# Kernel tuning notes

Hardware: AMD Instinct MI355X
Metric: run time of the kernel (lower is better)

The kernel has to match this reference:

```python
import jax, jax.numpy as jnp
import numpy as np

N, E, F_IN, H, L, G = 50000, 800000, 128, 256, 64, 500


def setup_inputs() -> dict:
    key = jax.random.key(0)
    ks = jax.random.split(key, 12)
    s = 0.02
    x = jax.random.normal(ks[0], (N, F_IN), dtype=jnp.float32)
    edge_index = jax.random.randint(ks[1], (2, E), 0, N, dtype=jnp.int64 if jax.config.jax_enable_x64 else jnp.int32)
    batch = jnp.sort(jax.random.randint(ks[2], (N,), 0, G, dtype=jnp.int32))
    return {
        "x": x,
        "edge_index": edge_index,
        "batch": batch,
        "num_graphs": G,
        "W1": jax.random.normal(ks[3], (F_IN, H), dtype=jnp.float32) * s,
        "b1": jnp.zeros((H,), dtype=jnp.float32),
        "W2": jax.random.normal(ks[4], (H, H), dtype=jnp.float32) * s,
        "b2": jnp.zeros((H,), dtype=jnp.float32),
        "Wmu": jax.random.normal(ks[5], (H, L), dtype=jnp.float32) * s,
        "bmu": jnp.zeros((L,), dtype=jnp.float32),
        "Wlv": jax.random.normal(ks[6], (H, L), dtype=jnp.float32) * s,
        "blv": jnp.zeros((L,), dtype=jnp.float32),
    }


def _gcn_norm(edge_index, n_nodes):
    # PyG GCNConv default: add self-loops, symmetric normalization D^-1/2 A_hat D^-1/2
    loop = jnp.arange(n_nodes, dtype=edge_index.dtype)
    src = jnp.concatenate([edge_index[0], loop])
    dst = jnp.concatenate([edge_index[1], loop])
    deg = jax.ops.segment_sum(jnp.ones_like(dst, dtype=jnp.float32), dst, num_segments=n_nodes)
    dinv = jnp.where(deg > 0, jax.lax.rsqrt(deg), 0.0)
    norm = dinv[src] * dinv[dst]  # [E + N]
    return src, dst, norm


def _gcn_conv(h, src, dst, norm, W, b, n_nodes):
    h = h @ W                              # [N, out]
    msg = norm[:, None] * h[src]           # gather + scale: [E+N, out]
    agg = jax.ops.segment_sum(msg, dst, num_segments=n_nodes)  # scatter-add
    return agg + b


def reference(x, edge_index, batch, num_graphs, W1, b1, W2, b2, Wmu, bmu, Wlv, blv):
    n_nodes = x.shape[0]
    src, dst, norm = _gcn_norm(edge_index, n_nodes)
    h = jax.nn.relu(_gcn_conv(x, src, dst, norm, W1, b1, n_nodes))
    h = jax.nn.relu(_gcn_conv(h, src, dst, norm, W2, b2, n_nodes))
    # global_mean_pool over batch ids
    sums = jax.ops.segment_sum(h, batch, num_segments=num_graphs)       # [G, H]
    cnt = jax.ops.segment_sum(jnp.ones((n_nodes,), h.dtype), batch, num_segments=num_graphs)
    h_graph = sums / jnp.maximum(cnt, 1.0)[:, None]
    mu = h_graph @ Wmu + bmu
    logvar = h_graph @ Wlv + blv
    return mu, logvar
```

## Files before the change

### kernel.cpp

```cpp
#include <hip/hip_runtime.h>
#include <hip/hip_fp16.h>

#define N_NODES 50000
#define N_EDGES 800000
#define F_IN_D  128
#define H_DIM   256
#define L_DIM   64
#define G_NUM   500

typedef unsigned int   u32;
typedef unsigned short u16;
typedef unsigned char  u8;
typedef __attribute__((ext_vector_type(8))) short short8;
typedef __attribute__((ext_vector_type(4))) float f32x4;
typedef __attribute__((ext_vector_type(2))) float f32x2;

#define BSHIFT 8
#define NBUCK ((N_NODES + 255) >> BSHIFT)
#define CUR_STRIDE 16
#define BIN_NB 512
#define EPB ((N_EDGES + BIN_NB - 1) / BIN_NB)
#define BUCK_CAP 8192

static __device__ __forceinline__ float bf2f(u16 u) {
    union { u32 i; float f; } x; x.i = ((u32)u) << 16; return x.f;
}
static __device__ __forceinline__ u16 f2bf(float f) {
    union { float f; u32 i; } x; x.f = f;
    u32 r = (x.i + 0x7fffu + ((x.i >> 16) & 1u)) >> 16;
    return (u16)r;
}
static __device__ __forceinline__ float edge_w(u32 e) {
    return __half2float(__ushort_as_half((u16)(e >> 16)));
}

static __device__ __forceinline__ u32 pack4_fp8(u32 a, u32 b) {
    u32 w = __builtin_amdgcn_cvt_pk_fp8_f32(bf2f((u16)(a & 0xffff)),
                                            bf2f((u16)(a >> 16)), 0, false);
    w = __builtin_amdgcn_cvt_pk_fp8_f32(bf2f((u16)(b & 0xffff)),
                                        bf2f((u16)(b >> 16)), w, true);
    return w;
}

static __device__ __forceinline__ u32 bswz_idx(int n, int k, int plane, int KS) {
    int n0g = n >> 6, nt = (n >> 4) & 3, lr = n & 15;
    int k0i = k >> 5, ks = k & 31, lq = ks >> 3, j = ks & 7;
    return ((u32)((((n0g * KS + k0i) * 2 + plane) * 4 + nt) * 64 + lq * 16 + lr)) * 8 + j;
}

#define NXQ (N_NODES * F_IN_D / 4)
#define NW1 (F_IN_D * H_DIM)
#define NW2 (H_DIM * H_DIM)
#define NB_SCAN  ((N_NODES + 255) / 256)
#define NB_CONV  ((NXQ + NW1 + NW2 + 255) / 256)

__global__ void prep_kernel(const int* __restrict__ src, const int* __restrict__ dst,
                            const int* __restrict__ batch, int* __restrict__ goff,
                            const float* __restrict__ x, u8* __restrict__ xq,
                            const float* __restrict__ W1, u16* __restrict__ w1swz,
                            const float* __restrict__ W2, u16* __restrict__ w2swz,
                            int* __restrict__ bcur, u32* __restrict__ binrec) {
    int b = blockIdx.x;
    if (b < BIN_NB) {
        __shared__ int lhist[NBUCK];
        __shared__ int lbase[NBUCK];
        int t = threadIdx.x;
        int e0 = b * EPB;
        int e1 = e0 + EPB; if (e1 > N_EDGES) e1 = N_EDGES;
        for (int i = t; i < NBUCK; i += 256) lhist[i] = 0;
        __syncthreads();
        for (int e = e0 + t; e < e1; e += 256)
            atomicAdd(&lhist[dst[e] >> BSHIFT], 1);
        __syncthreads();
        for (int i = t; i < NBUCK; i += 256) {
            int c = lhist[i];
            lbase[i] = i * BUCK_CAP + (c ? atomicAdd(&bcur[i * CUR_STRIDE], c) : 0);
            lhist[i] = 0;
        }
        __syncthreads();
        for (int e = e0 + t; e < e1; e += 256) {
            int d = dst[e], s = src[e];
            int bkt = d >> BSHIFT;
            int rank = atomicAdd(&lhist[bkt], 1);
            binrec[(size_t)lbase[bkt] + rank] = (u32)s | ((u32)(d & 255) << 16);
        }
    } else if (b < BIN_NB + NB_SCAN) {
        int i = (b - BIN_NB) * 256 + threadIdx.x;
        if (i >= N_NODES) return;
        int v = batch[i];
        if (i == 0) {
            for (int g = 0; g <= v; ++g) goff[g] = 0;
        } else {
            int p = batch[i - 1];
            for (int g = p + 1; g <= v; ++g) goff[g] = i;
        }
        if (i == N_NODES - 1) {
            for (int g = v + 1; g <= G_NUM; ++g) goff[g] = N_NODES;
        }
    } else {
        int i = (b - BIN_NB - NB_SCAN) * 256 + threadIdx.x;
        if (i < NXQ) {
            float4 v = *(const float4*)&x[(size_t)i * 4];
            u32 w = __builtin_amdgcn_cvt_pk_fp8_f32(v.x, v.y, 0, false);
            w = __builtin_amdgcn_cvt_pk_fp8_f32(v.z, v.w, w, true);
            *(u32*)&xq[(size_t)i * 4] = w;
        } else if (i < NXQ + NW1) {
            int idx = i - NXQ;
            int k = idx >> 8, n = idx & 255;
            float w = W1[idx];
            u16 h = f2bf(w);
            w1swz[bswz_idx(n, k, 0, F_IN_D / 32)] = h;
            w1swz[bswz_idx(n, k, 1, F_IN_D / 32)] = f2bf(w - bf2f(h));
        } else if (i < NXQ + NW1 + NW2) {
            int idx = i - NXQ - NW1;
            int k = idx >> 8, n = idx & 255;
            float w = W2[idx];
            u16 h = f2bf(w);
            w2swz[bswz_idx(n, k, 0, H_DIM / 32)] = h;
            w2swz[bswz_idx(n, k, 1, H_DIM / 32)] = f2bf(w - bf2f(h));
        }
    }
}

__global__ __launch_bounds__(256)
void cnt_scan_kernel(const int* __restrict__ bcur, const u32* __restrict__ binrec,
                     int* __restrict__ excl, int* __restrict__ partials,
                     float* __restrict__ dinv) {
    __shared__ int lh[256];
    __shared__ int sm[256];
    int b = blockIdx.x;
    int t = threadIdx.x;
    lh[t] = 0;
    __syncthreads();
    int s0 = b * BUCK_CAP;
    int s1 = s0 + bcur[b * CUR_STRIDE];
    for (int p = s0 + t; p < s1; p += 256)
        atomicAdd(&lh[(binrec[p] >> 16) & 255], 1);
    __syncthreads();
    int i = (b << BSHIFT) + t;
    int v = lh[t];
    sm[t] = v; __syncthreads();
    for (int off = 1; off < 256; off <<= 1) {
        int x = (t >= off) ? sm[t - off] : 0;
        __syncthreads();
        sm[t] += x;
        __syncthreads();
    }
    if (i < N_NODES) {
        excl[i] = sm[t] - v;
        dinv[i] = 1.0f / sqrtf((float)(v + 1));
    }
    if (t == 255) partials[b] = sm[255];
}

__global__ void scan_final_kernel(const int* __restrict__ excl, const int* __restrict__ partials,
                                  int* __restrict__ out, int n, int nb) {
    __shared__ int sm[256];
    int t = threadIdx.x;
    int v = (t < nb) ? partials[t] : 0;
    sm[t] = v; __syncthreads();
    for (int off = 1; off < 256; off <<= 1) {
        int x = (t >= off) ? sm[t - off] : 0;
        __syncthreads();
        sm[t] += x;
        __syncthreads();
    }
    int pre = (blockIdx.x > 0) ? sm[blockIdx.x - 1] : 0;
    int i = blockIdx.x * 256 + t;
    if (i < n) out[i] = excl[i] + pre;
    if (blockIdx.x == (unsigned)(nb - 1) && t == 0) out[n] = sm[nb - 1];
}

__global__ __launch_bounds__(256)
void place2_kernel(const int* __restrict__ rp, const int* __restrict__ bcur,
                   const u32* __restrict__ binrec, const float* __restrict__ dinv,
                   u32* __restrict__ csr) {
    __shared__ int ncur[256];
    int b = blockIdx.x;
    int t = threadIdx.x;
    int n0 = b << BSHIFT;
    int n1 = n0 + 256; if (n1 > N_NODES) n1 = N_NODES;
    if (n0 + t < n1) ncur[t] = rp[n0 + t];
    __syncthreads();
    int s0 = b * BUCK_CAP;
    int s1 = s0 + bcur[b * CUR_STRIDE];
    for (int p = s0 + t; p < s1; p += 256) {
        u32 r = binrec[p];
        int s = (int)(r & 0xffff);
        int pos = atomicAdd(&ncur[(r >> 16) & 255], 1);
        u32 w = (u32)__half_as_ushort(__float2half(dinv[s]));
        csr[pos] = (u32)s | (w << 16);
    }
}

__global__ __launch_bounds__(256)
void agg128_fp8_kernel(const u8* __restrict__ In, const float* __restrict__ dinv,
                       const int* __restrict__ rp, const u32* __restrict__ csr,
                       u16* __restrict__ Out) {
    int node = blockIdx.x * 4 + (threadIdx.x >> 6);
    int lane = threadIdx.x & 63;
    if (node >= N_NODES) return;
    int c = lane * 2;
    float di = dinv[node];
    int r0 = rp[node], r1 = rp[node + 1];
    u32 sv = *(const u16*)&In[(size_t)node * 128 + c];
    f32x2 s = __builtin_amdgcn_cvt_pk_f32_fp8(sv, false);
    float a0 = di * s.x;
    float a1 = di * s.y;
    int j = r0;
    for (; j + 8 <= r1; j += 8) {
        u32 e[8];
        u32 v[8];
#pragma unroll
        for (int q = 0; q < 8; ++q) e[q] = csr[j + q];
#pragma unroll
        for (int q = 0; q < 8; ++q) v[q] = *(const u16*)&In[(size_t)(e[q] & 0xffff) * 128 + c];
#pragma unroll
        for (int q = 0; q < 8; ++q) {
            float w = edge_w(e[q]);
            f32x2 p = __builtin_amdgcn_cvt_pk_f32_fp8(v[q], false);
            a0 = fmaf(w, p.x, a0);
            a1 = fmaf(w, p.y, a1);
        }
    }
    for (; j + 4 <= r1; j += 4) {
        u32 e[4];
        u32 v[4];
#pragma unroll
        for (int q = 0; q < 4; ++q) e[q] = csr[j + q];
#pragma unroll
        for (int q = 0; q < 4; ++q) v[q] = *(const u16*)&In[(size_t)(e[q] & 0xffff) * 128 + c];
#pragma unroll
        for (int q = 0; q < 4; ++q) {
            float w = edge_w(e[q]);
            f32x2 p = __builtin_amdgcn_cvt_pk_f32_fp8(v[q], false);
            a0 = fmaf(w, p.x, a0);
            a1 = fmaf(w, p.y, a1);
        }
    }
    for (; j < r1; ++j) {
        u32 e = csr[j];
        u32 v = *(const u16*)&In[(size_t)(e & 0xffff) * 128 + c];
        float w = edge_w(e);
        f32x2 p = __builtin_amdgcn_cvt_pk_f32_fp8(v, false);
        a0 = fmaf(w, p.x, a0);
        a1 = fmaf(w, p.y, a1);
    }
    u32 o = ((u32)f2bf(di * a1) << 16) | (u32)f2bf(di * a0);
    *(u32*)&Out[(size_t)node * 128 + c] = o;
}

__global__ __launch_bounds__(256)
void agg256_fp8_kernel(const u8* __restrict__ In, const float* __restrict__ dinv,
                       const int* __restrict__ rp, const u32* __restrict__ csr,
                       u16* __restrict__ Out) {
    int node = blockIdx.x * 4 + (threadIdx.x >> 6);
    int lane = threadIdx.x & 63;
    if (node >= N_NODES) return;
    int c = lane * 4;
    float di = dinv[node];
    int r0 = rp[node], r1 = rp[node + 1];
    u32 sv = *(const u32*)&In[(size_t)node * 256 + c];
    f32x2 s01 = __builtin_amdgcn_cvt_pk_f32_fp8(sv, false);
    f32x2 s23 = __builtin_amdgcn_cvt_pk_f32_fp8(sv, true);
    float a0 = di * s01.x;
    float a1 = di * s01.y;
    float a2 = di * s23.x;
    float a3 = di * s23.y;
    int j = r0;
    for (; j + 8 <= r1; j += 8) {
        u32 e[8];
        u32 v[8];
#pragma unroll
        for (int q = 0; q < 8; ++q) e[q] = csr[j + q];
#pragma unroll
        for (int q = 0; q < 8; ++q) v[q] = *(const u32*)&In[(size_t)(e[q] & 0xffff) * 256 + c];
#pragma unroll
        for (int q = 0; q < 8; ++q) {
            float w = edge_w(e[q]);
            f32x2 p0 = __builtin_amdgcn_cvt_pk_f32_fp8(v[q], false);
            f32x2 p1 = __builtin_amdgcn_cvt_pk_f32_fp8(v[q], true);
            a0 = fmaf(w, p0.x, a0);
            a1 = fmaf(w, p0.y, a1);
            a2 = fmaf(w, p1.x, a2);
            a3 = fmaf(w, p1.y, a3);
        }
    }
    for (; j + 4 <= r1; j += 4) {
        u32 e[4];
        u32 v[4];
#pragma unroll
        for (int q = 0; q < 4; ++q) e[q] = csr[j + q];
#pragma unroll
        for (int q = 0; q < 4; ++q) v[q] = *(const u32*)&In[(size_t)(e[q] & 0xffff) * 256 + c];
#pragma unroll
        for (int q = 0; q < 4; ++q) {
            float w = edge_w(e[q]);
            f32x2 p0 = __builtin_amdgcn_cvt_pk_f32_fp8(v[q], false);
            f32x2 p1 = __builtin_amdgcn_cvt_pk_f32_fp8(v[q], true);
            a0 = fmaf(w, p0.x, a0);
            a1 = fmaf(w, p0.y, a1);
            a2 = fmaf(w, p1.x, a2);
            a3 = fmaf(w, p1.y, a3);
        }
    }
    for (; j < r1; ++j) {
        u32 e = csr[j];
        u32 v = *(const u32*)&In[(size_t)(e & 0xffff) * 256 + c];
        float w = edge_w(e);
        f32x2 p0 = __builtin_amdgcn_cvt_pk_f32_fp8(v, false);
        f32x2 p1 = __builtin_amdgcn_cvt_pk_f32_fp8(v, true);
        a0 = fmaf(w, p0.x, a0);
        a1 = fmaf(w, p0.y, a1);
        a2 = fmaf(w, p1.x, a2);
        a3 = fmaf(w, p1.y, a3);
    }
    uint2 o;
    o.x = ((u32)f2bf(di * a1) << 16) | (u32)f2bf(di * a0);
    o.y = ((u32)f2bf(di * a3) << 16) | (u32)f2bf(di * a2);
    *(uint2*)&Out[(size_t)node * 256 + c] = o;
}

template<int K>
__global__ __launch_bounds__(256, 3)
void gemm1_kernel(const u16* __restrict__ A, const short8* __restrict__ Bswz,
                  const float* __restrict__ bias, u8* __restrict__ Out, int M) {
    const int KS = K / 32;
    __shared__ u16 cst[64][264];
    int tid  = threadIdx.x;
    int wave = tid >> 6, lane = tid & 63;
    int m0 = blockIdx.x * 64;
    int n0 = wave * 64;
    int lr = lane & 15;
    int lk = (lane >> 4) * 8;

    f32x4 acc[4][4];
#pragma unroll
    for (int i = 0; i < 4; ++i)
#pragma unroll
        for (int j = 0; j < 4; ++j) acc[i][j] = {0.f, 0.f, 0.f, 0.f};

    for (int k0i = 0; k0i < KS; ++k0i) {
        int k0 = k0i * 32;
        short8 a[4], bh[4], bl[4];
#pragma unroll
        for (int mt = 0; mt < 4; ++mt) {
            int m = m0 + mt * 16 + lr;
            if (m > M - 1) m = M - 1;
            a[mt] = *(const short8*)&A[(size_t)m * K + k0 + lk];
        }
        const short8* bp = Bswz + ((size_t)(wave * KS + k0i) * 8) * 64 + lane;
#pragma unroll
        for (int nt = 0; nt < 4; ++nt) {
            bh[nt] = bp[(size_t)nt * 64];
            bl[nt] = bp[(size_t)(4 + nt) * 64];
        }
#pragma unroll
        for (int mt = 0; mt < 4; ++mt)
#pragma unroll
            for (int nt = 0; nt < 4; ++nt) {
                acc[mt][nt] = __builtin_amdgcn_mfma_f32_16x16x32_bf16(a[mt], bh[nt], acc[mt][nt], 0, 0, 0);
                acc[mt][nt] = __builtin_amdgcn_mfma_f32_16x16x32_bf16(a[mt], bl[nt], acc[mt][nt], 0, 0, 0);
            }
    }

#pragma unroll
    for (int mt = 0; mt < 4; ++mt)
#pragma unroll
        for (int nt = 0; nt < 4; ++nt) {
            int col = n0 + nt * 16 + lr;
            float b = bias[col];
#pragma unroll
            for (int r = 0; r < 4; ++r) {
                int row = mt * 16 + (lane >> 4) * 4 + r;
                cst[row][col] = f2bf(fmaxf(acc[mt][nt][r] + b, 0.f));
            }
        }
    __syncthreads();
#pragma unroll
    for (int p = 0; p < 8; ++p) {
        int row = p * 8 + (tid >> 5);
        int c16 = (tid & 31) * 8;
        int m = m0 + row;
        if (m < M) {
            uint4 v = *(const uint4*)&cst[row][c16];
            uint2 o = make_uint2(pack4_fp8(v.x, v.y), pack4_fp8(v.z, v.w));
            *(uint2*)&Out[(size_t)m * 256 + c16] = o;
        }
    }
}

__global__ __launch_bounds__(256, 3)
void gemm2_pool_kernel(const u16* __restrict__ A, const short8* __restrict__ Bswz,
                       const float* __restrict__ bias, const int* __restrict__ batch,
                       float* __restrict__ pooled, int M) {
    const int K = H_DIM, KS = K / 32;
    __shared__ u16 cst[64][264];
    __shared__ int batch_s[64];
    int tid  = threadIdx.x;
    int wave = tid >> 6, lane = tid & 63;
    int m0 = blockIdx.x * 64;
    int n0 = wave * 64;
    int lr = lane & 15;
    int lk = (lane >> 4) * 8;

    f32x4 acc[4][4];
#pragma unroll
    for (int i = 0; i < 4; ++i)
#pragma unroll
        for (int j = 0; j < 4; ++j) acc[i][j] = {0.f, 0.f, 0.f, 0.f};

    for (int k0i = 0; k0i < KS; ++k0i) {
        int k0 = k0i * 32;
        short8 a[4], bh[4], bl[4];
#pragma unroll
        for (int mt = 0; mt < 4; ++mt) {
            int m = m0 + mt * 16 + lr;
            if (m > M - 1) m = M - 1;
            a[mt] = *(const short8*)&A[(size_t)m * K + k0 + lk];
        }
        const short8* bp = Bswz + ((size_t)(wave * KS + k0i) * 8) * 64 + lane;
#pragma unroll
        for (int nt = 0; nt < 4; ++nt) {
            bh[nt] = bp[(size_t)nt * 64];
            bl[nt] = bp[(size_t)(4 + nt) * 64];
        }
#pragma unroll
        for (int mt = 0; mt < 4; ++mt)
#pragma unroll
            for (int nt = 0; nt < 4; ++nt) {
                acc[mt][nt] = __builtin_amdgcn_mfma_f32_16x16x32_bf16(a[mt], bh[nt], acc[mt][nt], 0, 0, 0);
                acc[mt][nt] = __builtin_amdgcn_mfma_f32_16x16x32_bf16(a[mt], bl[nt], acc[mt][nt], 0, 0, 0);
            }
    }

    if (tid < 64) {
        int m = m0 + tid;
        batch_s[tid] = (m < M) ? batch[m] : -1;
    }
#pragma unroll
    for (int mt = 0; mt < 4; ++mt)
#pragma unroll
        for (int nt = 0; nt < 4; ++nt) {
            int col = n0 + nt * 16 + lr;
            float b = bias[col];
#pragma unroll
            for (int r = 0; r < 4; ++r) {
                int row = mt * 16 + (lane >> 4) * 4 + r;
                cst[row][col] = f2bf(fmaxf(acc[mt][nt][r] + b, 0.f));
            }
        }
    __syncthreads();

    int rows = M - m0; if (rows > 64) rows = 64;
    float s = 0.f;
    int gp = batch_s[0];
    for (int r = 0; r < rows; ++r) {
        int g = batch_s[r];
        if (g != gp) {
            atomicAdd(&pooled[(size_t)gp * H_DIM + tid], s);
            s = 0.f;
            gp = g;
        }
        s += bf2f(cst[r][tid]);
    }
    atomicAdd(&pooled[(size_t)gp * H_DIM + tid], s);
}

__global__ void head_kernel(const float* __restrict__ pooled, const int* __restrict__ goff,
                            const float* __restrict__ Wmu, const float* __restrict__ bmu,
                            const float* __restrict__ Wlv, const float* __restrict__ blv,
                            float* __restrict__ out) {
    __shared__ float hg[H_DIM];
    int g = blockIdx.x, l = threadIdx.x;
    float inv = 1.0f / fmaxf((float)(goff[g + 1] - goff[g]), 1.0f);
    for (int k = l; k < H_DIM; k += 64) hg[k] = pooled[(size_t)g * H_DIM + k] * inv;
    __syncthreads();
    float mu = bmu[l], lv = blv[l];
    for (int k = 0; k < H_DIM; ++k) {
        float h = hg[k];
        mu = fmaf(h, Wmu[k * L_DIM + l], mu);
        lv = fmaf(h, Wlv[k * L_DIM + l], lv);
    }
    out[(size_t)g * L_DIM + l] = mu;
    out[(size_t)G_NUM * L_DIM + (size_t)g * L_DIM + l] = lv;
}

extern "C" void kernel_launch(void* const* d_in, const int* in_sizes, int n_in,
                              void* d_out, int out_size, void* d_ws, size_t ws_size,
                              hipStream_t stream) {
    const float* x     = (const float*)d_in[0];
    const int*   ei    = (const int*)  d_in[1];
    const int*   batch = (const int*)  d_in[2];
    const float* W1  = (const float*)d_in[4];
    const float* b1  = (const float*)d_in[5];
    const float* W2  = (const float*)d_in[6];
    const float* b2  = (const float*)d_in[7];
    const float* Wmu = (const float*)d_in[8];
    const float* bmu = (const float*)d_in[9];
    const float* Wlv = (const float*)d_in[10];
    const float* blv = (const float*)d_in[11];
    const int* src = ei;
    const int* dst = ei + N_EDGES;

    char* ws = (char*)d_ws;
    size_t off = 0;
    auto alloc = [&](size_t bytes) -> void* {
        void* p = ws + off;
        off += (bytes + 255) & ~(size_t)255;
        return p;
    };
    float* pooled   = (float*)alloc((size_t)G_NUM * H_DIM * 4);
    int*   bcur     = (int*)alloc((size_t)NBUCK * CUR_STRIDE * 4);
    float* dinv     = (float*)alloc((size_t)N_NODES * 4);
    int*   row_ptr  = (int*)alloc((size_t)(N_NODES + 1) * 4);
    u32*   csr      = (u32*)alloc((size_t)N_EDGES * 4);
    u32*   binrec   = (u32*)alloc((size_t)NBUCK * BUCK_CAP * 4);
    int*   excl     = (int*)alloc((size_t)N_NODES * 4);
    int*   partials = (int*)alloc(256 * 4);
    int*   goff     = (int*)alloc((size_t)(G_NUM + 1) * 4);
    u8*    xq    = (u8*)alloc((size_t)N_NODES * F_IN_D);
    u16*   Xa    = (u16*)alloc((size_t)N_NODES * F_IN_D * 2);
    u8*    H8    = (u8*)alloc((size_t)N_NODES * H_DIM);
    u16*   Ha    = (u16*)alloc((size_t)N_NODES * H_DIM * 2);
    u16*   w1swz = (u16*)alloc((size_t)2 * F_IN_D * H_DIM * 2);
    u16*   w2swz = (u16*)alloc((size_t)2 * H_DIM * H_DIM * 2);
    (void)ws_size; (void)n_in; (void)in_sizes; (void)out_size;

    const int GEMM_NB = (N_NODES + 63) / 64;
    size_t zero_bytes = (size_t)((char*)(bcur + NBUCK * CUR_STRIDE) - (char*)pooled);

    hipMemsetAsync(pooled, 0, zero_bytes, stream);
    prep_kernel<<<BIN_NB + NB_SCAN + NB_CONV, 256, 0, stream>>>(
        src, dst, batch, goff, x, xq, W1, w1swz, W2, w2swz, bcur, binrec);
    cnt_scan_kernel<<<NBUCK, 256, 0, stream>>>(bcur, binrec, excl, partials, dinv);
    scan_final_kernel<<<NB_SCAN, 256, 0, stream>>>(excl, partials, row_ptr, N_NODES, NB_SCAN);
    place2_kernel<<<NBUCK, 256, 0, stream>>>(row_ptr, bcur, binrec, dinv, csr);

    agg128_fp8_kernel<<<(N_NODES + 3) / 4, 256, 0, stream>>>(xq, dinv, row_ptr, csr, Xa);
    gemm1_kernel<F_IN_D><<<GEMM_NB, 256, 0, stream>>>(Xa, (const short8*)w1swz, b1, H8, N_NODES);
    agg256_fp8_kernel<<<(N_NODES + 3) / 4, 256, 0, stream>>>(H8, dinv, row_ptr, csr, Ha);
    gemm2_pool_kernel<<<GEMM_NB, 256, 0, stream>>>(Ha, (const short8*)w2swz, b2, batch, pooled, N_NODES);

    head_kernel<<<G_NUM, 64, 0, stream>>>(pooled, goff, Wmu, bmu, Wlv, blv, (float*)d_out);
}
```

Baseline: 255.7 us.

## Fuse scan finalisation into CSR placement, widen gather unroll, store layer-2 aggregate as fp8

```diff
diff --git a/kernel.cpp b/kernel.cpp
--- a/kernel.cpp
+++ b/kernel.cpp
@@ -40,6 +40,24 @@
     w = __builtin_amdgcn_cvt_pk_fp8_f32(bf2f((u16)(b & 0xffff)),
                                         bf2f((u16)(b >> 16)), w, true);
     return w;
+}
+
+static __device__ __forceinline__ u32 pkbf16(float lo, float hi) {
+    u32 r;
+    asm("v_cvt_pk_bf16_f32 %0, %1, %2" : "=v"(r) : "v"(lo), "v"(hi));
+    return r;
+}
+static __device__ __forceinline__ short8 unpack8_fp8_bf16(uint2 v) {
+    f32x2 p0 = __builtin_amdgcn_cvt_pk_f32_fp8(v.x, false);
+    f32x2 p1 = __builtin_amdgcn_cvt_pk_f32_fp8(v.x, true);
+    f32x2 p2 = __builtin_amdgcn_cvt_pk_f32_fp8(v.y, false);
+    f32x2 p3 = __builtin_amdgcn_cvt_pk_f32_fp8(v.y, true);
+    union { u32 w[4]; short8 s; } u;
+    u.w[0] = pkbf16(p0.x, p0.y);
+    u.w[1] = pkbf16(p1.x, p1.y);
+    u.w[2] = pkbf16(p2.x, p2.y);
+    u.w[3] = pkbf16(p3.x, p3.y);
+    return u.s;
 }
 
 static __device__ __forceinline__ u32 bswz_idx(int n, int k, int plane, int KS) {
@@ -153,11 +171,16 @@
     if (t == 255) partials[b] = sm[255];
 }
 
-__global__ void scan_final_kernel(const int* __restrict__ excl, const int* __restrict__ partials,
-                                  int* __restrict__ out, int n, int nb) {
+__global__ __launch_bounds__(256)
+void place2_kernel(const int* __restrict__ excl, const int* __restrict__ partials,
+                   const int* __restrict__ bcur, const u32* __restrict__ binrec,
+                   const float* __restrict__ dinv,
+                   int* __restrict__ rp, u32* __restrict__ csr) {
     __shared__ int sm[256];
+    __shared__ int ncur[256];
+    int b = blockIdx.x;
     int t = threadIdx.x;
-    int v = (t < nb) ? partials[t] : 0;
+    int v = (t < NBUCK) ? partials[t] : 0;
     sm[t] = v; __syncthreads();
     for (int off = 1; off < 256; off <<= 1) {
         int x = (t >= off) ? sm[t - off] : 0;
@@ -165,22 +188,15 @@
         sm[t] += x;
         __syncthreads();
     }
-    int pre = (blockIdx.x > 0) ? sm[blockIdx.x - 1] : 0;
-    int i = blockIdx.x * 256 + t;
-    if (i < n) out[i] = excl[i] + pre;
-    if (blockIdx.x == (unsigned)(nb - 1) && t == 0) out[n] = sm[nb - 1];
-}
-
-__global__ __launch_bounds__(256)
-void place2_kernel(const int* __restrict__ rp, const int* __restrict__ bcur,
-                   const u32* __restrict__ binrec, const float* __restrict__ dinv,
-                   u32* __restrict__ csr) {
-    __shared__ int ncur[256];
-    int b = blockIdx.x;
-    int t = threadIdx.x;
+    int pre = (b > 0) ? sm[b - 1] : 0;
     int n0 = b << BSHIFT;
-    int n1 = n0 + 256; if (n1 > N_NODES) n1 = N_NODES;
-    if (n0 + t < n1) ncur[t] = rp[n0 + t];
+    int i = n0 + t;
+    if (i < N_NODES) {
+        int base = excl[i] + pre;
+        rp[i] = base;
+        ncur[t] = base;
+    }
+    if (b == NBUCK - 1 && t == 0) rp[N_NODES] = sm[NBUCK - 1];
     __syncthreads();
     int s0 = b * BUCK_CAP;
     int s1 = s0 + bcur[b * CUR_STRIDE];
@@ -208,15 +224,15 @@
     float a0 = di * s.x;
     float a1 = di * s.y;
     int j = r0;
-    for (; j + 8 <= r1; j += 8) {
-        u32 e[8];
-        u32 v[8];
-#pragma unroll
-        for (int q = 0; q < 8; ++q) e[q] = csr[j + q];
-#pragma unroll
-        for (int q = 0; q < 8; ++q) v[q] = *(const u16*)&In[(size_t)(e[q] & 0xffff) * 128 + c];
-#pragma unroll
-        for (int q = 0; q < 8; ++q) {
+    for (; j + 16 <= r1; j += 16) {
+        u32 e[16];
+        u32 v[16];
+#pragma unroll
+        for (int q = 0; q < 16; ++q) e[q] = csr[j + q];
+#pragma unroll
+        for (int q = 0; q < 16; ++q) v[q] = *(const u16*)&In[(size_t)(e[q] & 0xffff) * 128 + c];
+#pragma unroll
+        for (int q = 0; q < 16; ++q) {
             float w = edge_w(e[q]);
             f32x2 p = __builtin_amdgcn_cvt_pk_f32_fp8(v[q], false);
             a0 = fmaf(w, p.x, a0);
@@ -253,7 +269,7 @@
 __global__ __launch_bounds__(256)
 void agg256_fp8_kernel(const u8* __restrict__ In, const float* __restrict__ dinv,
                        const int* __restrict__ rp, const u32* __restrict__ csr,
-                       u16* __restrict__ Out) {
+                       u8* __restrict__ Out) {
     int node = blockIdx.x * 4 + (threadIdx.x >> 6);
     int lane = threadIdx.x & 63;
     if (node >= N_NODES) return;
@@ -268,15 +284,15 @@
     float a2 = di * s23.x;
     float a3 = di * s23.y;
     int j = r0;
-    for (; j + 8 <= r1; j += 8) {
-        u32 e[8];
-        u32 v[8];
-#pragma unroll
-        for (int q = 0; q < 8; ++q) e[q] = csr[j + q];
-#pragma unroll
-        for (int q = 0; q < 8; ++q) v[q] = *(const u32*)&In[(size_t)(e[q] & 0xffff) * 256 + c];
-#pragma unroll
-        for (int q = 0; q < 8; ++q) {
+    for (; j + 16 <= r1; j += 16) {
+        u32 e[16];
+        u32 v[16];
+#pragma unroll
+        for (int q = 0; q < 16; ++q) e[q] = csr[j + q];
+#pragma unroll
+        for (int q = 0; q < 16; ++q) v[q] = *(const u32*)&In[(size_t)(e[q] & 0xffff) * 256 + c];
+#pragma unroll
+        for (int q = 0; q < 16; ++q) {
             float w = edge_w(e[q]);
             f32x2 p0 = __builtin_amdgcn_cvt_pk_f32_fp8(v[q], false);
             f32x2 p1 = __builtin_amdgcn_cvt_pk_f32_fp8(v[q], true);
@@ -315,10 +331,9 @@
         a2 = fmaf(w, p1.x, a2);
         a3 = fmaf(w, p1.y, a3);
     }
-    uint2 o;
-    o.x = ((u32)f2bf(di * a1) << 16) | (u32)f2bf(di * a0);
-    o.y = ((u32)f2bf(di * a3) << 16) | (u32)f2bf(di * a2);
-    *(uint2*)&Out[(size_t)node * 256 + c] = o;
+    u32 o = __builtin_amdgcn_cvt_pk_fp8_f32(di * a0, di * a1, 0, false);
+    o = __builtin_amdgcn_cvt_pk_fp8_f32(di * a2, di * a3, o, true);
+    *(u32*)&Out[(size_t)node * 256 + c] = o;
 }
 
 template<int K>
@@ -391,7 +406,7 @@
 }
 
 __global__ __launch_bounds__(256, 3)
-void gemm2_pool_kernel(const u16* __restrict__ A, const short8* __restrict__ Bswz,
+void gemm2_pool_kernel(const u8* __restrict__ A, const short8* __restrict__ Bswz,
                        const float* __restrict__ bias, const int* __restrict__ batch,
                        float* __restrict__ pooled, int M) {
     const int K = H_DIM, KS = K / 32;
@@ -417,7 +432,8 @@
         for (int mt = 0; mt < 4; ++mt) {
             int m = m0 + mt * 16 + lr;
             if (m > M - 1) m = M - 1;
-            a[mt] = *(const short8*)&A[(size_t)m * K + k0 + lk];
+            uint2 araw = *(const uint2*)&A[(size_t)m * K + k0 + lk];
+            a[mt] = unpack8_fp8_bf16(araw);
         }
         const short8* bp = Bswz + ((size_t)(wave * KS + k0i) * 8) * 64 + lane;
 #pragma unroll
@@ -522,7 +538,7 @@
     u8*    xq    = (u8*)alloc((size_t)N_NODES * F_IN_D);
     u16*   Xa    = (u16*)alloc((size_t)N_NODES * F_IN_D * 2);
     u8*    H8    = (u8*)alloc((size_t)N_NODES * H_DIM);
-    u16*   Ha    = (u16*)alloc((size_t)N_NODES * H_DIM * 2);
+    u8*    Ha    = (u8*)alloc((size_t)N_NODES * H_DIM);
     u16*   w1swz = (u16*)alloc((size_t)2 * F_IN_D * H_DIM * 2);
     u16*   w2swz = (u16*)alloc((size_t)2 * H_DIM * H_DIM * 2);
     (void)ws_size; (void)n_in; (void)in_sizes; (void)out_size;
@@ -534,8 +550,7 @@
     prep_kernel<<<BIN_NB + NB_SCAN + NB_CONV, 256, 0, stream>>>(
         src, dst, batch, goff, x, xq, W1, w1swz, W2, w2swz, bcur, binrec);
     cnt_scan_kernel<<<NBUCK, 256, 0, stream>>>(bcur, binrec, excl, partials, dinv);
-    scan_final_kernel<<<NB_SCAN, 256, 0, stream>>>(excl, partials, row_ptr, N_NODES, NB_SCAN);
-    place2_kernel<<<NBUCK, 256, 0, stream>>>(row_ptr, bcur, binrec, dinv, csr);
+    place2_kernel<<<NBUCK, 256, 0, stream>>>(excl, partials, bcur, binrec, dinv, row_ptr, csr);
 
     agg128_fp8_kernel<<<(N_NODES + 3) / 4, 256, 0, stream>>>(xq, dinv, row_ptr, csr, Xa);
     gemm1_kernel<F_IN_D><<<GEMM_NB, 256, 0, stream>>>(Xa, (const short8*)w1swz, b1, H8, N_NODES);
```

New measurement: 249.8 us. 1.02x faster.
